# Performance work log

Measured on AMD Instinct MI355X. Metric: run time of the kernel, lower is better.

Reference implementation:

```python
import jax, jax.numpy as jnp
import numpy as np
from jax.lax import associative_scan

D_H = 512

def _binary_operator(e_i, e_j):
    a_i, kv_i = e_i
    a_j, kv_j = e_j
    return (a_j * a_i, a_j * kv_i + kv_j)

def setup_inputs() -> dict:
    key = jax.random.key(0)
    x = jax.random.normal(key, (4, 8192, 3 * D_H), dtype=jnp.float32)
    return {"x": x}

def reference(x):
    d_h = x.shape[-1] // 3
    inp = jnp.tanh(x[:, :, :d_h])
    gates = jax.nn.sigmoid(x[:, :, d_h:])
    input_gate, output_gate = jnp.split(gates, 2, axis=-1)
    forget_gate = 1.0 - input_gate
    # diagonal linear recurrence h_t = f_t * h_{t-1} + i_t * x_t via associative scan
    _, hidden_state = associative_scan(_binary_operator, (forget_gate, inp * input_gate), axis=1)
    return jnp.tanh(hidden_state) * output_gate
```

## Files before the change

### kernel.cpp

```cpp
#include <hip/hip_runtime.h>


#define B_   4
#define T_   8192
#define DH_  512
#define ROW_ 1536
#define C_   512
#define TC_  16

typedef float f32x4 __attribute__((ext_vector_type(4)));

__device__ __forceinline__ float rcp_f(float x) {
    return __builtin_amdgcn_rcpf(x);
}
__device__ __forceinline__ float sigmoid_f(float x) {
    return rcp_f(1.0f + __expf(-x));
}
__device__ __forceinline__ float tanh_f(float x) {
    return 1.0f - 2.0f * rcp_f(__expf(2.0f * x) + 1.0f);
}

__global__ void k_partials(const float* __restrict__ x,
                           float* __restrict__ agg_a,
                           float* __restrict__ agg_kv) {
    const int c = blockIdx.x;
    const int b = blockIdx.y;
    const int d = threadIdx.x << 2;
    const float* xb = x + ((size_t)b * T_ + (size_t)c * TC_) * ROW_;

    float A[4]  = {1.f, 1.f, 1.f, 1.f};
    float KV[4] = {0.f, 0.f, 0.f, 0.f};
#pragma unroll
    for (int i = 0; i < TC_; ++i) {
        const float* r = xb + (size_t)i * ROW_;
        const f32x4 xi = *(const f32x4*)(r + d);
        const f32x4 gi = *(const f32x4*)(r + DH_ + d);
#pragma unroll
        for (int j = 0; j < 4; ++j) {
            const float s  = sigmoid_f(gi[j]);
            const float f  = 1.0f - s;
            const float iv = tanh_f(xi[j]) * s;
            A[j]  = f * A[j];
            KV[j] = fmaf(f, KV[j], iv);
        }
    }
    const size_t idx = ((size_t)b * C_ + c) * DH_ + d;
    f32x4 Av  = {A[0],  A[1],  A[2],  A[3]};
    f32x4 KVv = {KV[0], KV[1], KV[2], KV[3]};
    *(f32x4*)(agg_a + idx)  = Av;
    *(f32x4*)(agg_kv + idx) = KVv;
}

__global__ void k_scan(const float* __restrict__ agg_a,
                       const float* __restrict__ agg_kv,
                       float* __restrict__ h0) {
    __shared__ float sa[C_];
    __shared__ float sk[C_];
    const int d = blockIdx.x;
    const int b = blockIdx.y;
    const int c = threadIdx.x;

    const size_t idx = ((size_t)b * C_ + c) * DH_ + d;
    float am = agg_a[idx];
    float km = agg_kv[idx];
    sa[c] = am;
    sk[c] = km;
    __syncthreads();

    for (int o = 1; o < C_; o <<= 1) {
        float ap = 1.f, kp = 0.f;
        if (c >= o) { ap = sa[c - o]; kp = sk[c - o]; }
        __syncthreads();
        km = fmaf(am, kp, km);
        am = am * ap;
        sa[c] = am;
        sk[c] = km;
        __syncthreads();
    }

    h0[idx] = (c == 0) ? 0.f : sk[c - 1];
}

__global__ void k_apply(const float* __restrict__ x,
                        const float* __restrict__ h0buf,
                        float* __restrict__ out) {
    const int c = blockIdx.x;
    const int b = blockIdx.y;
    const int d = threadIdx.x << 2;

    float h[4];
    const f32x4 hv = *(const f32x4*)(h0buf + ((size_t)b * C_ + c) * DH_ + d);
#pragma unroll
    for (int j = 0; j < 4; ++j) h[j] = hv[j];

    const float* xb = x + ((size_t)b * T_ + (size_t)c * TC_) * ROW_;
    float* ob = out + ((size_t)b * T_ + (size_t)c * TC_) * DH_;

#pragma unroll 8
    for (int i = 0; i < TC_; ++i) {
        const float* r = xb + (size_t)i * ROW_;
        const f32x4 xi = *(const f32x4*)(r + d);
        const f32x4 gi = *(const f32x4*)(r + DH_ + d);
        const f32x4 go = *(const f32x4*)(r + 2 * DH_ + d);
        f32x4 o;
#pragma unroll
        for (int j = 0; j < 4; ++j) {
            const float s  = sigmoid_f(gi[j]);
            const float f  = 1.0f - s;
            const float iv = tanh_f(xi[j]) * s;
            h[j] = fmaf(f, h[j], iv);
            o[j] = tanh_f(h[j]) * sigmoid_f(go[j]);
        }
        __builtin_nontemporal_store(o, (f32x4*)(ob + (size_t)i * DH_ + d));
    }
}

__global__ void k_seq(const float* __restrict__ x, float* __restrict__ out) {
    const int b = blockIdx.x;
    const int d4 = threadIdx.x << 2;
    const float* xb = x + (size_t)b * T_ * ROW_;
    float* ob = out + (size_t)b * T_ * DH_;
    float h[4] = {0.f, 0.f, 0.f, 0.f};
    for (int i = 0; i < T_; ++i) {
        const float* r = xb + (size_t)i * ROW_;
        const f32x4 xi = *(const f32x4*)(r + d4);
        const f32x4 gi = *(const f32x4*)(r + DH_ + d4);
        const f32x4 go = *(const f32x4*)(r + 2 * DH_ + d4);
        f32x4 o;
#pragma unroll
        for (int j = 0; j < 4; ++j) {
            const float s  = sigmoid_f(gi[j]);
            const float f  = 1.0f - s;
            const float iv = tanh_f(xi[j]) * s;
            h[j] = fmaf(f, h[j], iv);
            o[j] = tanh_f(h[j]) * sigmoid_f(go[j]);
        }
        *(f32x4*)(ob + (size_t)i * DH_ + d4) = o;
    }
}

extern "C" void kernel_launch(void* const* d_in, const int* in_sizes, int n_in,
                              void* d_out, int out_size, void* d_ws, size_t ws_size,
                              hipStream_t stream) {
    const float* x = (const float*)d_in[0];
    float* out = (float*)d_out;

    const size_t n_agg = (size_t)B_ * C_ * DH_;
    if (ws_size < 3 * n_agg * sizeof(float)) {
        hipLaunchKernelGGL(k_seq, dim3(B_), dim3(DH_ / 4), 0, stream, x, out);
        return;
    }

    float* agg_a  = (float*)d_ws;
    float* agg_kv = agg_a  + n_agg;
    float* h0     = agg_kv + n_agg;

    const dim3 grid(C_, B_);
    const dim3 blk(DH_ / 4);
    hipLaunchKernelGGL(k_partials, grid, blk, 0, stream, x, agg_a, agg_kv);
    hipLaunchKernelGGL(k_scan, dim3(DH_, B_), dim3(C_), 0, stream,
                       agg_a, agg_kv, h0);
    hipLaunchKernelGGL(k_apply, grid, blk, 0, stream, x, h0, out);
}
```

Measured before the change: 332.7 us.

## Fuse three-pass chunked scan into single-pass decoupled-lookback kernel

Replaces the partials, scan and apply kernels with one kernel using decoupled lookback. Each block publishes its chunk aggregate and, once known, its inclusive state, and spin-waits on predecessors through status flags. Each chunk's input and gate data are read again while still likely in cache, and two launches plus the separate scan pass go away. In exchange it adds a memset, spin-waiting whose correctness depends on blocks being scheduled in order, and serial lookback latency across 512 chunks.

```diff
diff --git a/kernel.cpp b/kernel.cpp
--- a/kernel.cpp
+++ b/kernel.cpp
@@ -20,17 +20,21 @@
     return 1.0f - 2.0f * rcp_f(__expf(2.0f * x) + 1.0f);
 }
 
-__global__ void k_partials(const float* __restrict__ x,
-                           float* __restrict__ agg_a,
-                           float* __restrict__ agg_kv) {
+__global__ __launch_bounds__(128, 4)
+void k_lookback(const float* __restrict__ x,
+                float* __restrict__ out,
+                float* __restrict__ agg_a,
+                float* __restrict__ agg_kv,
+                float* __restrict__ h_incl,
+                int* __restrict__ status) {
     const int c = blockIdx.x;
     const int b = blockIdx.y;
     const int d = threadIdx.x << 2;
     const float* xb = x + ((size_t)b * T_ + (size_t)c * TC_) * ROW_;
 
-    float A[4]  = {1.f, 1.f, 1.f, 1.f};
-    float KV[4] = {0.f, 0.f, 0.f, 0.f};
-#pragma unroll
+    float A[4] = {1.f, 1.f, 1.f, 1.f};
+    float K[4] = {0.f, 0.f, 0.f, 0.f};
+#pragma unroll 8
     for (int i = 0; i < TC_; ++i) {
         const float* r = xb + (size_t)i * ROW_;
         const f32x4 xi = *(const f32x4*)(r + d);
@@ -40,62 +44,71 @@
             const float s  = sigmoid_f(gi[j]);
             const float f  = 1.0f - s;
             const float iv = tanh_f(xi[j]) * s;
-            A[j]  = f * A[j];
-            KV[j] = fmaf(f, KV[j], iv);
+            A[j] *= f;
+            K[j] = fmaf(f, K[j], iv);
         }
     }
-    const size_t idx = ((size_t)b * C_ + c) * DH_ + d;
-    f32x4 Av  = {A[0],  A[1],  A[2],  A[3]};
-    f32x4 KVv = {KV[0], KV[1], KV[2], KV[3]};
-    *(f32x4*)(agg_a + idx)  = Av;
-    *(f32x4*)(agg_kv + idx) = KVv;
-}
 
-__global__ void k_scan(const float* __restrict__ agg_a,
-                       const float* __restrict__ agg_kv,
-                       float* __restrict__ h0) {
-    __shared__ float sa[C_];
-    __shared__ float sk[C_];
-    const int d = blockIdx.x;
-    const int b = blockIdx.y;
-    const int c = threadIdx.x;
+    const size_t cbase = ((size_t)b * C_ + c) * DH_ + d;
+#pragma unroll
+    for (int j = 0; j < 4; ++j) {
+        __hip_atomic_store(agg_a  + cbase + j, A[j], __ATOMIC_RELAXED, __HIP_MEMORY_SCOPE_AGENT);
+        __hip_atomic_store(agg_kv + cbase + j, K[j], __ATOMIC_RELAXED, __HIP_MEMORY_SCOPE_AGENT);
+    }
+    __syncthreads();
+    if (threadIdx.x == 0)
+        __hip_atomic_store(status + b * C_ + c, 1, __ATOMIC_RELEASE, __HIP_MEMORY_SCOPE_AGENT);
 
-    const size_t idx = ((size_t)b * C_ + c) * DH_ + d;
-    float am = agg_a[idx];
-    float km = agg_kv[idx];
-    sa[c] = am;
-    sk[c] = km;
-    __syncthreads();
-
-    for (int o = 1; o < C_; o <<= 1) {
-        float ap = 1.f, kp = 0.f;
-        if (c >= o) { ap = sa[c - o]; kp = sk[c - o]; }
-        __syncthreads();
-        km = fmaf(am, kp, km);
-        am = am * ap;
-        sa[c] = am;
-        sk[c] = km;
-        __syncthreads();
+    float h0[4] = {0.f, 0.f, 0.f, 0.f};
+    if (c > 0) {
+        float Ap[4] = {1.f, 1.f, 1.f, 1.f};
+        float Kp[4] = {0.f, 0.f, 0.f, 0.f};
+        int cc = c - 1;
+        while (cc >= 0) {
+            const int* sp = status + b * C_ + cc;
+            int st;
+            do {
+                st = __hip_atomic_load(sp, __ATOMIC_ACQUIRE, __HIP_MEMORY_SCOPE_AGENT);
+            } while (st == 0);
+            const size_t pb = ((size_t)b * C_ + cc) * DH_ + d;
+            if (st == 2) {
+#pragma unroll
+                for (int j = 0; j < 4; ++j) {
+                    const float hi = __hip_atomic_load(h_incl + pb + j, __ATOMIC_RELAXED, __HIP_MEMORY_SCOPE_AGENT);
+                    h0[j] = fmaf(Ap[j], hi, Kp[j]);
+                }
+                break;
+            } else {
+#pragma unroll
+                for (int j = 0; j < 4; ++j) {
+                    const float ac = __hip_atomic_load(agg_a  + pb + j, __ATOMIC_RELAXED, __HIP_MEMORY_SCOPE_AGENT);
+                    const float kc = __hip_atomic_load(agg_kv + pb + j, __ATOMIC_RELAXED, __HIP_MEMORY_SCOPE_AGENT);
+                    Kp[j] = fmaf(Ap[j], kc, Kp[j]);
+                    Ap[j] *= ac;
+                }
+                --cc;
+            }
+        }
+        if (cc < 0) {
+#pragma unroll
+            for (int j = 0; j < 4; ++j) h0[j] = Kp[j];
+        }
     }
 
-    h0[idx] = (c == 0) ? 0.f : sk[c - 1];
-}
-
-__global__ void k_apply(const float* __restrict__ x,
-                        const float* __restrict__ h0buf,
-                        float* __restrict__ out) {
-    const int c = blockIdx.x;
-    const int b = blockIdx.y;
-    const int d = threadIdx.x << 2;
+#pragma unroll
+    for (int j = 0; j < 4; ++j) {
+        const float hi = fmaf(A[j], h0[j], K[j]);
+        __hip_atomic_store(h_incl + cbase + j, hi, __ATOMIC_RELAXED, __HIP_MEMORY_SCOPE_AGENT);
+    }
+    __syncthreads();
+    if (threadIdx.x == 0)
+        __hip_atomic_store(status + b * C_ + c, 2, __ATOMIC_RELEASE, __HIP_MEMORY_SCOPE_AGENT);
 
     float h[4];
-    const f32x4 hv = *(const f32x4*)(h0buf + ((size_t)b * C_ + c) * DH_ + d);
 #pragma unroll
-    for (int j = 0; j < 4; ++j) h[j] = hv[j];
+    for (int j = 0; j < 4; ++j) h[j] = h0[j];
 
-    const float* xb = x + ((size_t)b * T_ + (size_t)c * TC_) * ROW_;
     float* ob = out + ((size_t)b * T_ + (size_t)c * TC_) * DH_;
-
 #pragma unroll 8
     for (int i = 0; i < TC_; ++i) {
         const float* r = xb + (size_t)i * ROW_;
@@ -146,19 +159,19 @@
     float* out = (float*)d_out;
 
     const size_t n_agg = (size_t)B_ * C_ * DH_;
-    if (ws_size < 3 * n_agg * sizeof(float)) {
+    const size_t need  = 3 * n_agg * sizeof(float) + (size_t)B_ * C_ * sizeof(int);
+    if (ws_size < need) {
         hipLaunchKernelGGL(k_seq, dim3(B_), dim3(DH_ / 4), 0, stream, x, out);
         return;
     }
 
     float* agg_a  = (float*)d_ws;
     float* agg_kv = agg_a  + n_agg;
-    float* h0     = agg_kv + n_agg;
+    float* h_incl = agg_kv + n_agg;
+    int*   status = (int*)(h_incl + n_agg);
 
-    const dim3 grid(C_, B_);
-    const dim3 blk(DH_ / 4);
-    hipLaunchKernelGGL(k_partials, grid, blk, 0, stream, x, agg_a, agg_kv);
-    hipLaunchKernelGGL(k_scan, dim3(DH_, B_), dim3(C_), 0, stream,
-                       agg_a, agg_kv, h0);
-    hipLaunchKernelGGL(k_apply, grid, blk, 0, stream, x, h0, out);
+    hipMemsetAsync(status, 0, (size_t)B_ * C_ * sizeof(int), stream);
+
+    hipLaunchKernelGGL(k_lookback, dim3(C_, B_), dim3(DH_ / 4), 0, stream,
+                       x, out, agg_a, agg_kv, h_incl, status);
 }
```

After: 1.309 ms. 293% more time.
